# Kernel tuning notes

Hardware: AMD Instinct MI355X
Metric: run time of the kernel (lower is better)

Reference implementation:

```python
import jax, jax.numpy as jnp
import numpy as np

N, K, C, OUT = 2048, 14, 512, 512
SCALE = 4.0
BN_EPS = 1e-5


def _edge_lists(k):
    # pairs i<j with i,j != k-1 and adj[i,j] > 0 (adj is fully connected ones)
    ei, ej = [], []
    for i in range(k - 1):
        for j in range(i + 1, k - 1):
            ei.append(i)
            ej.append(j)
    return np.asarray(ei, np.int32), np.asarray(ej, np.int32)


def setup_inputs() -> dict:
    key = jax.random.key(0)
    k0, k1, k2, k3 = jax.random.split(key, 4)
    ei, ej = _edge_lists(K)
    std = 0.02
    return {
        "inputs": jax.random.normal(k0, (N, K, C), dtype=jnp.float32),
        "adj": jnp.ones((K, K), dtype=jnp.float32),
        "edge_i": jnp.asarray(ei),
        "edge_j": jnp.asarray(ej),
        "gamma": jnp.ones((C,), dtype=jnp.float32),
        "beta": jnp.zeros((C,), dtype=jnp.float32),
        "w_direct": jax.random.normal(k1, (C,), dtype=jnp.float32) * std,
        "W_merged": jax.random.normal(k2, (OUT, C), dtype=jnp.float32) * std,
        "W_orig": jax.random.normal(k3, (OUT, C), dtype=jnp.float32) * std,
    }


def reference(inputs, adj, edge_i, edge_j, gamma, beta, w_direct, W_merged, W_orig):
    n, k, c = inputs.shape
    # --- learn_adj ---
    global_feat = inputs[:, k - 1 : k, :]                      # [N,1,c]
    distances = jnp.abs(inputs - global_feat)                  # [N,k,c]
    # pairwise gaps only on the static edge list (i<j, non-global, adj>0)
    gap = 15.0 * (distances[:, edge_i, :] - distances[:, edge_j, :])  # [N,E,c]
    # BatchNorm1d over channel c, batch stats over (N, E), biased variance
    mean = jnp.mean(gap, axis=(0, 1))
    var = jnp.mean(jnp.square(gap - mean), axis=(0, 1))
    bn = (gap - mean) * (gamma / jnp.sqrt(var + BN_EPS)) + beta        # [N,E,c]
    a = jax.nn.sigmoid(SCALE * jnp.einsum("nec,c->ne", bn, w_direct))  # [N,E]
    adj2 = jnp.ones((n, k, k), dtype=inputs.dtype)
    adj2 = adj2.at[:, edge_i, edge_j].set(2.0 * a)
    adj2 = adj2.at[:, edge_j, edge_i].set(2.0 * (1.0 - a))
    new_adj = adj2 * adj[None, :, :]
    norm = jnp.sum(jnp.abs(new_adj), axis=2, keepdims=True)    # L1 row norm
    new_adj = new_adj / jnp.maximum(norm, 1e-12)
    # --- graph conv ---
    agg = jnp.einsum("nij,njc->nic", new_adj, inputs)          # [N,k,c]
    merged = jax.nn.relu(jnp.einsum("nkc,oc->nko", agg, W_merged))
    original = jnp.einsum("nkc,oc->nko", inputs, W_orig)
    return merged + original
```

## Files before the change

kernel.cpp:

```cpp
#include <hip/hip_runtime.h>
#include <stdint.h>

#define K_NODES 14
#define C_DIM   512
#define OUT_DIM 512
#define N_EDGE  78

typedef float  f32x4  __attribute__((ext_vector_type(4)));
typedef __bf16 bf16x8 __attribute__((ext_vector_type(8)));

__device__ __forceinline__ unsigned short f2bf(float f) {
    unsigned int u = __builtin_bit_cast(unsigned int, f);
    unsigned int r = (u + 0x7fffu + ((u >> 16) & 1u)) >> 16;
    return (unsigned short)r;
}
__device__ __forceinline__ float bf2f(unsigned short s) {
    return __builtin_bit_cast(float, (unsigned int)s << 16);
}

__device__ __forceinline__ void async16(const void* g, void* l) {
    __builtin_amdgcn_global_load_lds(
        (const __attribute__((address_space(1))) unsigned int*)g,
        (__attribute__((address_space(3))) unsigned int*)l, 16, 0, 0);
}

__global__ __launch_bounds__(1024) void stats_partial(
    const float* __restrict__ x, float* __restrict__ part,
    unsigned short* __restrict__ xbf,
    const float* __restrict__ Wm, const float* __restrict__ Wo,
    unsigned short* __restrict__ wmbf, unsigned short* __restrict__ wobf)
{
    int t  = threadIdx.x;
    int q  = t & 127;
    int sn = t >> 7;
    int n  = blockIdx.x * 8 + sn;
    size_t base = (size_t)n * K_NODES * C_DIM + q * 4;

    f32x4 g = *(const f32x4*)(x + base + 13 * C_DIM);
    ushort4 gb; gb.x=f2bf(g.x); gb.y=f2bf(g.y); gb.z=f2bf(g.z); gb.w=f2bf(g.w);
    *(ushort4*)(xbf + base + 13 * C_DIM) = gb;

    float S10=0,S11=0,S12=0,S13=0, S20=0,S21=0,S22=0,S23=0, Sw0=0,Sw1=0,Sw2=0,Sw3=0;
    #pragma unroll
    for (int k = 0; k < 13; ++k) {
        f32x4 v = *(const f32x4*)(x + base + k * C_DIM);
        ushort4 vb; vb.x=f2bf(v.x); vb.y=f2bf(v.y); vb.z=f2bf(v.z); vb.w=f2bf(v.w);
        *(ushort4*)(xbf + base + k * C_DIM) = vb;
        float wk = (float)(12 - 2 * k);
        float d0=fabsf(v.x-g.x), d1=fabsf(v.y-g.y), d2=fabsf(v.z-g.z), d3=fabsf(v.w-g.w);
        S10+=d0; S11+=d1; S12+=d2; S13+=d3;
        S20+=d0*d0; S21+=d1*d1; S22+=d2*d2; S23+=d3*d3;
        Sw0+=wk*d0; Sw1+=wk*d1; Sw2+=wk*d2; Sw3+=wk*d3;
    }
    f32x4 as = (f32x4){15.f*Sw0, 15.f*Sw1, 15.f*Sw2, 15.f*Sw3};
    f32x4 aq = (f32x4){225.f*(13.f*S20 - S10*S10), 225.f*(13.f*S21 - S11*S11),
                       225.f*(13.f*S22 - S12*S12), 225.f*(13.f*S23 - S13*S13)};

    __shared__ f32x4 redS[8][128];
    __shared__ f32x4 redQ[8][128];
    redS[sn][q] = as;
    redQ[sn][q] = aq;
    __syncthreads();
    if (sn == 0) {
        f32x4 s = redS[0][q], z = redQ[0][q];
        #pragma unroll
        for (int r = 1; r < 8; ++r) { s += redS[r][q]; z += redQ[r][q]; }
        *(f32x4*)(part + (size_t)blockIdx.x * 1024 + q * 4)       = s;
        *(f32x4*)(part + (size_t)blockIdx.x * 1024 + 512 + q * 4) = z;
    }
    int i0 = blockIdx.x * 1024 + t;
    wmbf[i0] = f2bf(Wm[i0]);
    wobf[i0] = f2bf(Wo[i0]);
}

__global__ __launch_bounds__(256) void finalize_stats(
    const float* __restrict__ part, float inv_ne,
    const float* __restrict__ gamma, const float* __restrict__ beta,
    const float* __restrict__ wdir, float* __restrict__ u, float* __restrict__ bpart)
{
    int lane = threadIdx.x & 63;
    int wv   = threadIdx.x >> 6;
    int c    = blockIdx.x * 64 + lane;
    float s = 0.f, q = 0.f;
    #pragma unroll 8
    for (int r = wv; r < 256; r += 4) {
        s += part[(size_t)r * 1024 + c];
        q += part[(size_t)r * 1024 + 512 + c];
    }
    __shared__ float shs[4][64], shq[4][64];
    shs[wv][lane] = s; shq[wv][lane] = q;
    __syncthreads();
    if (wv == 0) {
        s = shs[0][lane] + shs[1][lane] + shs[2][lane] + shs[3][lane];
        q = shq[0][lane] + shq[1][lane] + shq[2][lane] + shq[3][lane];
        float mean = s * inv_ne;
        float var  = q * inv_ne - mean * mean;
        float sc   = gamma[c] / sqrtf(var + 1e-5f);
        u[c] = sc * wdir[c];
        float b = (beta[c] - mean * sc) * wdir[c];
        #pragma unroll
        for (int off = 1; off < 64; off <<= 1) b += __shfl_xor(b, off, 64);
        if (lane == 0) bpart[blockIdx.x] = b;
    }
}

__global__ __launch_bounds__(256) void fuse_graph(
    const unsigned short* __restrict__ xbf, const float* __restrict__ adj,
    const int* __restrict__ ei, const int* __restrict__ ej,
    const float* __restrict__ u, const float* __restrict__ bpart,
    unsigned short* __restrict__ aggbf)
{
    __shared__ float WL[2][196];
    __shared__ float Dp[2][2][13];
    __shared__ float invL[2][14];
    int wv = threadIdx.x >> 6, lane = threadIdx.x & 63;
    int sp = wv >> 1;
    int h  = wv & 1;
    int n  = blockIdx.x * 2 + sp;
    size_t base = (size_t)n * K_NODES * C_DIM + h * 256 + lane * 4;

    float xf[K_NODES][4];
    #pragma unroll
    for (int k = 0; k < K_NODES; ++k) {
        uint2 raw = *(const uint2*)(xbf + base + k * C_DIM);
        xf[k][0]=bf2f(raw.x&0xffff); xf[k][1]=bf2f(raw.x>>16);
        xf[k][2]=bf2f(raw.y&0xffff); xf[k][3]=bf2f(raw.y>>16);
    }
    f32x4 uv = *(const f32x4*)(u + h * 256 + lane * 4);

    #pragma unroll
    for (int k = 0; k < 13; ++k) {
        float p = fabsf(xf[k][0]-xf[13][0])*uv.x + fabsf(xf[k][1]-xf[13][1])*uv.y
                + fabsf(xf[k][2]-xf[13][2])*uv.z + fabsf(xf[k][3]-xf[13][3])*uv.w;
        #pragma unroll
        for (int off = 1; off < 64; off <<= 1) p += __shfl_xor(p, off, 64);
        if (lane == 0) Dp[sp][h][k] = p;
    }
    __syncthreads();

    if (h == 0) {
        float bc = 0.f;
        #pragma unroll
        for (int b8 = 0; b8 < 8; ++b8) bc += bpart[b8];
        for (int e = lane; e < N_EDGE; e += 64) {
            int ii = ei[e], jj = ej[e];
            float Di = Dp[sp][0][ii] + Dp[sp][1][ii];
            float Dj = Dp[sp][0][jj] + Dp[sp][1][jj];
            float z = 4.0f * (15.f * (Di - Dj) + bc);
            float a = 1.f / (1.f + expf(-z));
            WL[sp][ii * K_NODES + jj] = adj[ii * K_NODES + jj] * (2.f * a);
            WL[sp][jj * K_NODES + ii] = adj[jj * K_NODES + ii] * (2.f * (1.f - a));
        }
    } else {
        for (int idx = lane; idx < K_NODES * K_NODES; idx += 64) {
            int i = idx / K_NODES, j = idx - i * K_NODES;
            if (i == j || i == 13 || j == 13) WL[sp][idx] = adj[idx];
        }
    }
    __syncthreads();
    if (h == 0 && lane < K_NODES) {
        float s = 0.f;
        #pragma unroll
        for (int j = 0; j < K_NODES; ++j) s += fabsf(WL[sp][lane * K_NODES + j]);
        invL[sp][lane] = 1.f / fmaxf(s, 1e-12f);
    }
    __syncthreads();

    #pragma unroll
    for (int i = 0; i < K_NODES; ++i) {
        float s0=0.f,s1=0.f,s2=0.f,s3=0.f;
        #pragma unroll
        for (int j = 0; j < K_NODES; ++j) {
            float w = WL[sp][i * K_NODES + j];
            s0 += w*xf[j][0]; s1 += w*xf[j][1]; s2 += w*xf[j][2]; s3 += w*xf[j][3];
        }
        float wi = invL[sp][i];
        uint2 r;
        r.x = (unsigned int)f2bf(s0*wi) | ((unsigned int)f2bf(s1*wi) << 16);
        r.y = (unsigned int)f2bf(s2*wi) | ((unsigned int)f2bf(s3*wi) << 16);
        *(uint2*)(aggbf + base + i * C_DIM) = r;
    }
}

#define TM 128
#define TN 128
#define BK 64

__global__ __launch_bounds__(256) void gemm_fused(
    const unsigned short* __restrict__ Aagg, const unsigned short* __restrict__ Axin,
    const unsigned short* __restrict__ Bwm,  const unsigned short* __restrict__ Bwo,
    float* __restrict__ out)
{
    __shared__ unsigned short lA[2][TM * BK];
    __shared__ unsigned short lB[2][TN * BK];
    int tid  = threadIdx.x;
    int lane = tid & 63;
    int wave = tid >> 6;
    int wr = wave >> 1, wc = wave & 1;
    int bm = blockIdx.x * TM;
    int bn = blockIdx.y * TN;

    f32x4 acc[4][4];
    #pragma unroll
    for (int i = 0; i < 4; ++i)
        #pragma unroll
        for (int j = 0; j < 4; ++j) acc[i][j] = (f32x4){0.f, 0.f, 0.f, 0.f};

    int lrow = lane & 15;
    int xorv = lane & 7;
    int srow  = tid >> 3;
    int lcu   = ((tid & 7) ^ (srow & 7)) * 8;

#define STAGE(buf, Ap, Bp, kb)                                              \
    _Pragma("unroll")                                                        \
    for (int it = 0; it < 4; ++it) {                                         \
        int row = it * 32 + srow;                                            \
        async16((Ap) + (size_t)(bm + row) * C_DIM + (kb) + lcu,              \
                &lA[buf][(it * 256 + wave * 64) * 8]);                       \
        async16((Bp) + (size_t)(bn + row) * C_DIM + (kb) + lcu,              \
                &lB[buf][(it * 256 + wave * 64) * 8]);                       \
    }

    STAGE(0, Aagg, Bwm, 0);
    __syncthreads();

    #pragma unroll
    for (int ph = 0; ph < 16; ++ph) {
        const int cur = ph & 1;
        if (ph < 15) {
            const unsigned short* Ap = ((ph + 1) < 8) ? Aagg : Axin;
            const unsigned short* Bp = ((ph + 1) < 8) ? Bwm  : Bwo;
            STAGE(cur ^ 1, Ap, Bp, ((ph + 1) & 7) * BK);
        }
        #pragma unroll
        for (int ks = 0; ks < 2; ++ks) {
            int pchunk = ((ks * 4 + (lane >> 4)) ^ xorv) * 8;
            bf16x8 af[4], bfr[4];
            #pragma unroll
            for (int i = 0; i < 4; ++i)
                af[i] = *(const bf16x8*)&lA[cur][(wr * 64 + i * 16 + lrow) * BK + pchunk];
            #pragma unroll
            for (int j = 0; j < 4; ++j)
                bfr[j] = *(const bf16x8*)&lB[cur][(wc * 64 + j * 16 + lrow) * BK + pchunk];
            #pragma unroll
            for (int i = 0; i < 4; ++i)
                #pragma unroll
                for (int j = 0; j < 4; ++j)
                    acc[i][j] = __builtin_amdgcn_mfma_f32_16x16x32_bf16(
                        af[i], bfr[j], acc[i][j], 0, 0, 0);
        }
        if (ph == 7) {
            #pragma unroll
            for (int i = 0; i < 4; ++i)
                #pragma unroll
                for (int j = 0; j < 4; ++j)
                    #pragma unroll
                    for (int r = 0; r < 4; ++r)
                        acc[i][j][r] = fmaxf(acc[i][j][r], 0.f);
        }
        __syncthreads();
    }
#undef STAGE

    int orow0 = bm + wr * 64 + (lane >> 4) * 4;
    int ocol0 = bn + wc * 64 + (lane & 15);
    #pragma unroll
    for (int i = 0; i < 4; ++i)
        #pragma unroll
        for (int j = 0; j < 4; ++j)
            #pragma unroll
            for (int r = 0; r < 4; ++r)
                out[(size_t)(orow0 + i * 16 + r) * OUT_DIM + (ocol0 + j * 16)] = acc[i][j][r];
}

extern "C" void kernel_launch(void* const* d_in, const int* in_sizes, int n_in,
                              void* d_out, int out_size, void* d_ws, size_t ws_size,
                              hipStream_t stream)
{
    const float* x     = (const float*)d_in[0];
    const float* adj   = (const float*)d_in[1];
    const int*   ei    = (const int*)d_in[2];
    const int*   ej    = (const int*)d_in[3];
    const float* gamma = (const float*)d_in[4];
    const float* beta  = (const float*)d_in[5];
    const float* wdir  = (const float*)d_in[6];
    const float* Wm    = (const float*)d_in[7];
    const float* Wo    = (const float*)d_in[8];
    float* out = (float*)d_out;

    int N = in_sizes[0] / (K_NODES * C_DIM);
    int M = N * K_NODES;

    float* ws_f   = (float*)d_ws;
    float* u      = ws_f + 1024;
    float* bpart  = ws_f + 1536;
    float* part   = ws_f + 2048;
    char*  wsb    = (char*)d_ws;
    size_t off    = (size_t)(2048 + 256 * 1024) * sizeof(float);
    unsigned short* wmbf  = (unsigned short*)(wsb + off);  off += (size_t)OUT_DIM * C_DIM * 2;
    unsigned short* wobf  = (unsigned short*)(wsb + off);  off += (size_t)OUT_DIM * C_DIM * 2;
    unsigned short* xbf   = (unsigned short*)(wsb + off);  off += (size_t)M * C_DIM * 2;
    unsigned short* aggbf = (unsigned short*)(wsb + off);

    float inv_ne = 1.0f / ((float)N * (float)N_EDGE);

    hipLaunchKernelGGL(stats_partial, dim3(N / 8), dim3(1024), 0, stream,
                       x, part, xbf, Wm, Wo, wmbf, wobf);
    hipLaunchKernelGGL(finalize_stats, dim3(8), dim3(256), 0, stream,
                       part, inv_ne, gamma, beta, wdir, u, bpart);
    hipLaunchKernelGGL(fuse_graph, dim3(N / 2), dim3(256), 0, stream,
                       xbf, adj, ei, ej, u, bpart, aggbf);
    hipLaunchKernelGGL(gemm_fused, dim3(M / TM, OUT_DIM / TN), dim3(256), 0, stream,
                       aggbf, xbf, wmbf, wobf, out);
}
```

Baseline: 183.3 us.

## Triple-buffer GEMM with BK=32 and fine-grained vmcnt waits

Restructures the fused GEMM main loop from a double-buffered BK=64 pipeline into a triple-buffered BK=32 pipeline that keeps two stages of async global-to-LDS loads in flight. Full __syncthreads are replaced with explicit s_waitcnt vmcnt/lgkmcnt plus s_barrier, and MFMA sections are wrapped in s_setprio. The LDS swizzle is changed to suit 32-wide rows, and launch bounds request 3 blocks per CU. This aims to hide global load latency and raise occupancy, at the cost of more barriers per K step and hand-tuned wait counts that must exactly match the number of outstanding loads.

```diff
diff --git a/kernel.cpp b/kernel.cpp
--- a/kernel.cpp
+++ b/kernel.cpp
@@ -184,15 +184,15 @@
 
 #define TM 128
 #define TN 128
-#define BK 64
-
-__global__ __launch_bounds__(256) void gemm_fused(
+#define BK 32
+
+__global__ __launch_bounds__(256, 3) void gemm_fused(
     const unsigned short* __restrict__ Aagg, const unsigned short* __restrict__ Axin,
     const unsigned short* __restrict__ Bwm,  const unsigned short* __restrict__ Bwo,
     float* __restrict__ out)
 {
-    __shared__ unsigned short lA[2][TM * BK];
-    __shared__ unsigned short lB[2][TN * BK];
+    __shared__ unsigned short lA[3][TM * BK];
+    __shared__ unsigned short lB[3][TN * BK];
     int tid  = threadIdx.x;
     int lane = tid & 63;
     int wave = tid >> 6;
@@ -207,49 +207,57 @@
         for (int j = 0; j < 4; ++j) acc[i][j] = (f32x4){0.f, 0.f, 0.f, 0.f};
 
     int lrow = lane & 15;
-    int xorv = lane & 7;
-    int srow  = tid >> 3;
-    int lcu   = ((tid & 7) ^ (srow & 7)) * 8;
-
-#define STAGE(buf, Ap, Bp, kb)                                              \
-    _Pragma("unroll")                                                        \
-    for (int it = 0; it < 4; ++it) {                                         \
-        int row = it * 32 + srow;                                            \
-        async16((Ap) + (size_t)(bm + row) * C_DIM + (kb) + lcu,              \
-                &lA[buf][(it * 256 + wave * 64) * 8]);                       \
-        async16((Bp) + (size_t)(bn + row) * C_DIM + (kb) + lcu,              \
-                &lB[buf][(it * 256 + wave * 64) * 8]);                       \
+    int kc   = lane >> 4;
+    int pcs  = (kc ^ ((lrow >> 1) & 3)) * 8;
+    int srow = lane >> 2;
+    int scol = lane & 3;
+    int lc   = scol ^ ((srow >> 1) & 3);
+    size_t goff0 = (size_t)(wave * 16 + srow) * C_DIM + lc * 8;
+    size_t goff1 = goff0 + (size_t)64 * C_DIM;
+
+#define STAGE(buf, Ap, Bp, kb)                                               \
+    {                                                                         \
+        async16((Ap) + (size_t)bm * C_DIM + (kb) + goff0,                     \
+                &lA[buf][(wave * 16) * BK]);                                  \
+        async16((Ap) + (size_t)bm * C_DIM + (kb) + goff1,                     \
+                &lA[buf][(64 + wave * 16) * BK]);                             \
+        async16((Bp) + (size_t)bn * C_DIM + (kb) + goff0,                     \
+                &lB[buf][(wave * 16) * BK]);                                  \
+        async16((Bp) + (size_t)bn * C_DIM + (kb) + goff1,                     \
+                &lB[buf][(64 + wave * 16) * BK]);                             \
     }
 
     STAGE(0, Aagg, Bwm, 0);
-    __syncthreads();
-
-    #pragma unroll
-    for (int ph = 0; ph < 16; ++ph) {
-        const int cur = ph & 1;
-        if (ph < 15) {
-            const unsigned short* Ap = ((ph + 1) < 8) ? Aagg : Axin;
-            const unsigned short* Bp = ((ph + 1) < 8) ? Bwm  : Bwo;
-            STAGE(cur ^ 1, Ap, Bp, ((ph + 1) & 7) * BK);
-        }
-        #pragma unroll
-        for (int ks = 0; ks < 2; ++ks) {
-            int pchunk = ((ks * 4 + (lane >> 4)) ^ xorv) * 8;
+    STAGE(1, Aagg, Bwm, BK);
+    asm volatile("s_waitcnt vmcnt(4)" ::: "memory");
+    __builtin_amdgcn_s_barrier();
+
+    #pragma unroll 32
+    for (int t = 0; t < 32; ++t) {
+        if (t + 2 < 32) {
+            const unsigned short* Ap = ((t + 2) < 16) ? Aagg : Axin;
+            const unsigned short* Bp = ((t + 2) < 16) ? Bwm  : Bwo;
+            STAGE((t + 2) % 3, Ap, Bp, ((t + 2) & 15) * BK);
+        }
+        {
+            const int buf = t % 3;
             bf16x8 af[4], bfr[4];
             #pragma unroll
             for (int i = 0; i < 4; ++i)
-                af[i] = *(const bf16x8*)&lA[cur][(wr * 64 + i * 16 + lrow) * BK + pchunk];
+                af[i] = *(const bf16x8*)&lA[buf][(wr * 64 + i * 16 + lrow) * BK + pcs];
             #pragma unroll
             for (int j = 0; j < 4; ++j)
-                bfr[j] = *(const bf16x8*)&lB[cur][(wc * 64 + j * 16 + lrow) * BK + pchunk];
+                bfr[j] = *(const bf16x8*)&lB[buf][(wc * 64 + j * 16 + lrow) * BK + pcs];
+            __builtin_amdgcn_s_setprio(1);
             #pragma unroll
             for (int i = 0; i < 4; ++i)
                 #pragma unroll
                 for (int j = 0; j < 4; ++j)
                     acc[i][j] = __builtin_amdgcn_mfma_f32_16x16x32_bf16(
                         af[i], bfr[j], acc[i][j], 0, 0, 0);
-        }
-        if (ph == 7) {
+            __builtin_amdgcn_s_setprio(0);
+        }
+        if (t == 15) {
             #pragma unroll
             for (int i = 0; i < 4; ++i)
                 #pragma unroll
@@ -258,7 +266,11 @@
                     for (int r = 0; r < 4; ++r)
                         acc[i][j][r] = fmaxf(acc[i][j][r], 0.f);
         }
-        __syncthreads();
+        asm volatile("s_waitcnt lgkmcnt(0)" ::: "memory");
+        __builtin_amdgcn_sched_barrier(0);
+        if (t < 30)      asm volatile("s_waitcnt vmcnt(4)" ::: "memory");
+        else             asm volatile("s_waitcnt vmcnt(0)" ::: "memory");
+        if (t < 31) __builtin_amdgcn_s_barrier();
     }
 #undef STAGE
 
```

Result: no change. 185.5 us (+1.2%).
